# Kernel optimization log

Hardware: AMD Instinct MI355X
Metric: run time of the kernel (lower is better)

Reference implementation:

```python
import jax, jax.numpy as jnp
import numpy as np

B, T, C, H = 4, 2048, 1024, 16
HS = C // H  # head size 64
LN_EPS = 1e-5


def setup_inputs() -> dict:
    key = jax.random.key(0)
    ks = jax.random.split(key, 14)
    s = lambda fan_in: 1.0 / np.sqrt(fan_in)
    return {
        "x": jax.random.normal(ks[0], (B, T, C), jnp.float32),
        # weights stored [in, out] (transposed vs torch nn.Linear) for y = x @ W + b
        "c_attn_w": jax.random.normal(ks[1], (C, 3 * C), jnp.float32) * s(C),
        "c_attn_b": jnp.zeros((3 * C,), jnp.float32),
        "c_proj_w": jax.random.normal(ks[2], (C, C), jnp.float32) * s(C),
        "c_proj_b": jnp.zeros((C,), jnp.float32),
        "fc_w": jax.random.normal(ks[3], (C, 4 * C), jnp.float32) * s(C),
        "fc_b": jnp.zeros((4 * C,), jnp.float32),
        "proj_w": jax.random.normal(ks[4], (4 * C, C), jnp.float32) * s(4 * C),
        "proj_b": jnp.zeros((C,), jnp.float32),
        "ln1_g": jnp.ones((C,), jnp.float32),
        "ln1_b": jnp.zeros((C,), jnp.float32),
        "ln2_g": jnp.ones((C,), jnp.float32),
        "ln2_b": jnp.zeros((C,), jnp.float32),
    }


def layer_norm(x, g, b):
    mu = jnp.mean(x, axis=-1, keepdims=True)
    var = jnp.var(x, axis=-1, keepdims=True)
    return (x - mu) * jax.lax.rsqrt(var + LN_EPS) * g + b


def attention(x, c_attn_w, c_attn_b, c_proj_w, c_proj_b):
    Bs, Ts, Cs = x.shape
    qkv = x @ c_attn_w + c_attn_b  # (B,T,3C)
    q, k, v = jnp.split(qkv, 3, axis=-1)
    q = q.reshape(Bs, Ts, H, HS).transpose(0, 2, 1, 3)  # (B,H,T,hs)
    k = k.reshape(Bs, Ts, H, HS).transpose(0, 2, 1, 3)
    v = v.reshape(Bs, Ts, H, HS).transpose(0, 2, 1, 3)
    wei = jnp.einsum("bhqd,bhkd->bhqk", q, k) * (1.0 / np.sqrt(HS))
    causal = jnp.tril(jnp.ones((Ts, Ts), bool))
    wei = jnp.where(causal, wei, -jnp.inf)
    wei = jax.nn.softmax(wei, axis=-1)
    out = jnp.einsum("bhqk,bhkd->bhqd", wei, v)
    out = out.transpose(0, 2, 1, 3).reshape(Bs, Ts, Cs)
    return out @ c_proj_w + c_proj_b


def mlp(x, fc_w, fc_b, proj_w, proj_b):
    h = jax.nn.gelu(x @ fc_w + fc_b, approximate=True)
    return h @ proj_w + proj_b


def reference(x, c_attn_w, c_attn_b, c_proj_w, c_proj_b, fc_w, fc_b, proj_w, proj_b, ln1_g, ln1_b, ln2_g, ln2_b):
    x = x + attention(layer_norm(x, ln1_g, ln1_b), c_attn_w, c_attn_b, c_proj_w, c_proj_b)
    out = x + mlp(layer_norm(x, ln2_g, ln2_b), fc_w, fc_b, proj_w, proj_b)
    return out
```

## Files before the change

### kernel.cpp

```cpp
#include <hip/hip_runtime.h>

typedef unsigned short u16;
typedef __attribute__((ext_vector_type(8))) short bf16x8;
typedef __attribute__((ext_vector_type(4))) float f32x4;

#define SC_LOG2E 0.18033688011112043f
#define MB_LOG2E 17.31234049066756f

__device__ __forceinline__ float b2f(u16 u) {
  union { unsigned int i; float f; } v; v.i = ((unsigned int)u) << 16; return v.f;
}
__device__ __forceinline__ u16 f2b(float f) {
  unsigned int x = __float_as_uint(f);
  unsigned int r = (x + 0x7fffu + ((x >> 16) & 1u)) >> 16;
  return (u16)r;
}

#define GLOAD_LDS16(g, l)                                                              \
  __builtin_amdgcn_global_load_lds((const __attribute__((address_space(1))) void*)(g), \
                                   (__attribute__((address_space(3))) void*)(l), 16, 0, 0)

__global__ __launch_bounds__(256) void transpose_cast_kernel(const float* __restrict__ in,
                                                             u16* __restrict__ out,
                                                             int K, int N) {
  __shared__ float tile[64][65];
  const int tid = threadIdx.x;
  const int n0 = blockIdx.x * 64, k0 = blockIdx.y * 64;
#pragma unroll
  for (int it = 0; it < 4; ++it) {
    int lin = it * 256 + tid;
    int r = lin >> 4, c4 = (lin & 15) * 4;
    float4 v = *(const float4*)&in[(size_t)(k0 + r) * N + n0 + c4];
    tile[r][c4 + 0] = v.x; tile[r][c4 + 1] = v.y;
    tile[r][c4 + 2] = v.z; tile[r][c4 + 3] = v.w;
  }
  __syncthreads();
#pragma unroll
  for (int it = 0; it < 2; ++it) {
    int lin = it * 256 + tid;
    int r = lin >> 3, c8 = (lin & 7) * 8;
    u16 tmp[8];
#pragma unroll
    for (int j = 0; j < 8; ++j) tmp[j] = f2b(tile[c8 + j][r]);
    *(uint4*)&out[(size_t)(n0 + r) * K + k0 + c8] = *(const uint4*)tmp;
  }
}

__global__ __launch_bounds__(256) void transpose_v_kernel(const u16* __restrict__ qkv,
                                                          u16* __restrict__ vt) {
  __shared__ float tl[64][65];
  const int tid = threadIdx.x;
  const int bh = blockIdx.y, b = bh >> 4, h = bh & 15;
  const int t0 = blockIdx.x * 64;
  const int voff = 2048 + h * 64;
#pragma unroll
  for (int it = 0; it < 2; ++it) {
    int lin = it * 256 + tid;
    int tt = lin >> 3, d8 = (lin & 7) * 8;
    uint4 v = *(const uint4*)&qkv[((size_t)b * 2048 + t0 + tt) * 3072 + voff + d8];
    const u16* p = (const u16*)&v;
#pragma unroll
    for (int j = 0; j < 8; ++j) tl[tt][d8 + j] = b2f(p[j]);
  }
  __syncthreads();
#pragma unroll
  for (int it = 0; it < 2; ++it) {
    int lin = it * 256 + tid;
    int d = lin >> 3, t8 = (lin & 7) * 8;
    u16 tmp[8];
#pragma unroll
    for (int j = 0; j < 8; ++j) tmp[j] = f2b(tl[t8 + j][d]);
    *(uint4*)&vt[((size_t)bh * 64 + d) * 2048 + t0 + t8] = *(const uint4*)tmp;
  }
}

template <bool INF32>
__global__ __launch_bounds__(256) void ln_kernel(const void* __restrict__ xv,
                                                 const float* __restrict__ g,
                                                 const float* __restrict__ b,
                                                 u16* __restrict__ o, int C) {
  const int row = blockIdx.x, tid = threadIdx.x;
  const int wave = tid >> 6, lane = tid & 63;
  const int base = tid * 4;
  float f[4];
  if (INF32) {
    float4 v = *(const float4*)((const float*)xv + (size_t)row * C + base);
    f[0] = v.x; f[1] = v.y; f[2] = v.z; f[3] = v.w;
  } else {
    ushort4 v = *(const ushort4*)((const u16*)xv + (size_t)row * C + base);
    f[0] = b2f(v.x); f[1] = b2f(v.y); f[2] = b2f(v.z); f[3] = b2f(v.w);
  }
  float s = f[0] + f[1] + f[2] + f[3];
  float q = f[0] * f[0] + f[1] * f[1] + f[2] * f[2] + f[3] * f[3];
#pragma unroll
  for (int off = 1; off < 64; off <<= 1) {
    s += __shfl_xor(s, off);
    q += __shfl_xor(q, off);
  }
  __shared__ float reds[4], redq[4];
  if (lane == 0) { reds[wave] = s; redq[wave] = q; }
  __syncthreads();
  float S = reds[0] + reds[1] + reds[2] + reds[3];
  float Q = redq[0] + redq[1] + redq[2] + redq[3];
  const float inv = 1.0f / (float)C;
  float mean = S * inv;
  float var = Q * inv - mean * mean;
  float rs = rsqrtf(var + 1e-5f);
  float4 gv = *(const float4*)&g[base];
  float4 bv = *(const float4*)&b[base];
  ushort4 ov;
  ov.x = f2b((f[0] - mean) * rs * gv.x + bv.x);
  ov.y = f2b((f[1] - mean) * rs * gv.y + bv.y);
  ov.z = f2b((f[2] - mean) * rs * gv.z + bv.z);
  ov.w = f2b((f[3] - mean) * rs * gv.w + bv.w);
  *(ushort4*)&o[(size_t)row * C + base] = ov;
}

__device__ __forceinline__ float gelu_fn(float v) {
  float a = 0.7978845608028654f * __builtin_fmaf(0.044715f * v * v, v, v);
  float t = __builtin_amdgcn_exp2f(a * -2.8853900817779268f);
  return v * __builtin_amdgcn_rcpf(1.0f + t);
}

template <bool GELU, int RESMODE, bool OUTF32>
__global__ __launch_bounds__(256) void gemm_kernel(const u16* __restrict__ A,
                                                   const u16* __restrict__ Bt,
                                                   const float* __restrict__ bias,
                                                   const void* __restrict__ res,
                                                   void* __restrict__ Cv,
                                                   int M, int N, int K) {
  __shared__ u16 As[128 * 64];
  __shared__ u16 Bs[128 * 64];
  const int tid = threadIdx.x;
  const int wave = tid >> 6, lane = tid & 63;
  const int lhi = lane >> 4, llo = lane & 15;
  const int sw = llo & 7;
  const int m0 = blockIdx.x * 128, n0 = blockIdx.y * 128;
  const int wr = (wave >> 1) * 64, wc = (wave & 1) * 64;

  f32x4 acc[4][4] = {};

  for (int k0 = 0; k0 < K; k0 += 64) {
#pragma unroll
    for (int p = 0; p < 4; ++p) {
      int s = p * 256 + tid;
      int r = s >> 3;
      int c = ((s & 7) ^ (r & 7)) * 8;
      GLOAD_LDS16(A + (size_t)(m0 + r) * K + k0 + c, As + s * 8);
      GLOAD_LDS16(Bt + (size_t)(n0 + r) * K + k0 + c, Bs + s * 8);
    }
    __syncthreads();
#pragma unroll
    for (int kk = 0; kk < 2; ++kk) {
      const int cp = ((kk * 4 + lhi) ^ sw) * 8;
      bf16x8 af[4], bf[4];
#pragma unroll
      for (int i = 0; i < 4; ++i)
        af[i] = *(const bf16x8*)&As[(wr + i * 16 + llo) * 64 + cp];
#pragma unroll
      for (int j = 0; j < 4; ++j)
        bf[j] = *(const bf16x8*)&Bs[(wc + j * 16 + llo) * 64 + cp];
#pragma unroll
      for (int i = 0; i < 4; ++i)
#pragma unroll
        for (int j = 0; j < 4; ++j)
          acc[i][j] = __builtin_amdgcn_mfma_f32_16x16x32_bf16(af[i], bf[j], acc[i][j], 0, 0, 0);
    }
    __syncthreads();
  }

#pragma unroll
  for (int i = 0; i < 4; ++i) {
    int row = m0 + wr + i * 16 + lhi * 4;
#pragma unroll
    for (int j = 0; j < 4; ++j) {
      int col = n0 + wc + j * 16 + llo;
      float bv = bias[col];
#pragma unroll
      for (int r = 0; r < 4; ++r) {
        float v = acc[i][j][r] + bv;
        if (GELU) v = gelu_fn(v);
        size_t idx = (size_t)(row + r) * N + col;
        if (RESMODE == 1) v += b2f(((const u16*)res)[idx]);
        if (RESMODE == 2) v += ((const float*)res)[idx];
        if (OUTF32) ((float*)Cv)[idx] = v;
        else ((u16*)Cv)[idx] = f2b(v);
      }
    }
  }
}

template <bool GELU>
__global__ __launch_bounds__(512, 2) void gemm256_kernel(const u16* __restrict__ A,
                                                         const u16* __restrict__ Bt,
                                                         const float* __restrict__ bias,
                                                         u16* __restrict__ Cv,
                                                         int M, int N, int K) {
  __shared__ u16 As[2][256 * 64];
  __shared__ u16 Bs[2][256 * 64];
  const int tid = threadIdx.x;
  const int wave = tid >> 6, lane = tid & 63;
  const int lhi = lane >> 4, llo = lane & 15;
  const int sw = llo & 7;
  const int m0 = blockIdx.x * 256, n0 = blockIdx.y * 256;
  const int wr = (wave >> 2) * 128, wc = (wave & 3) * 64;

  f32x4 acc[8][4] = {};
  const int nkt = K >> 6;

  auto stage = [&](int b, int kt) {
    const int k0 = kt * 64;
#pragma unroll
    for (int p = 0; p < 4; ++p) {
      int s = p * 512 + tid;
      int r = s >> 3;
      int c = ((s & 7) ^ (r & 7)) * 8;
      GLOAD_LDS16(A + (size_t)(m0 + r) * K + k0 + c, &As[b][s * 8]);
      GLOAD_LDS16(Bt + (size_t)(n0 + r) * K + k0 + c, &Bs[b][s * 8]);
    }
  };

  stage(0, 0);
  stage(1, 1);
  asm volatile("s_waitcnt vmcnt(8)" ::: "memory");
  __builtin_amdgcn_s_barrier();

  int cur = 0;
  for (int kt = 0; kt < nkt; ++kt) {
#pragma unroll
    for (int kk = 0; kk < 2; ++kk) {
      const int cp = ((kk * 4 + lhi) ^ sw) * 8;
      bf16x8 af[8], bf[4];
#pragma unroll
      for (int i = 0; i < 8; ++i)
        af[i] = *(const bf16x8*)&As[cur][(wr + i * 16 + llo) * 64 + cp];
#pragma unroll
      for (int j = 0; j < 4; ++j)
        bf[j] = *(const bf16x8*)&Bs[cur][(wc + j * 16 + llo) * 64 + cp];
      __builtin_amdgcn_s_setprio(1);
#pragma unroll
      for (int i = 0; i < 8; ++i)
#pragma unroll
        for (int j = 0; j < 4; ++j)
          acc[i][j] = __builtin_amdgcn_mfma_f32_16x16x32_bf16(af[i], bf[j], acc[i][j], 0, 0, 0);
      __builtin_amdgcn_s_setprio(0);
    }
    asm volatile("s_waitcnt lgkmcnt(0)" ::: "memory");
    __builtin_amdgcn_s_barrier();
    if (kt + 2 < nkt) {
      stage(cur, kt + 2);
      asm volatile("s_waitcnt vmcnt(8)" ::: "memory");
      __builtin_amdgcn_s_barrier();
    } else if (kt + 1 < nkt) {
      asm volatile("s_waitcnt vmcnt(0)" ::: "memory");
      __builtin_amdgcn_s_barrier();
    }
    cur ^= 1;
  }

#pragma unroll
  for (int i = 0; i < 8; ++i) {
    int row = m0 + wr + i * 16 + lhi * 4;
#pragma unroll
    for (int j = 0; j < 4; ++j) {
      int col = n0 + wc + j * 16 + llo;
      float bv = bias[col];
#pragma unroll
      for (int r = 0; r < 4; ++r) {
        float v = acc[i][j][r] + bv;
        if (GELU) v = gelu_fn(v);
        Cv[(size_t)(row + r) * N + col] = f2b(v);
      }
    }
  }
}

__global__ __launch_bounds__(512, 4) void attn_kernel(const u16* __restrict__ qkv,
                                                      const u16* __restrict__ vt,
                                                      u16* __restrict__ out) {
  __shared__ u16 Ks[64 * 68];
  __shared__ u16 Vs[64 * 68];
  __shared__ u16 Ps[128 * 68];
  const int tid = threadIdx.x;
  const int wave = tid >> 6, lane = tid & 63;
  const int lhi = lane >> 4, llo = lane & 15;
  const int pr = blockIdx.x;
  const int bh = blockIdx.y;
  const int b = bh >> 4, h = bh & 15;
  const size_t rowbase = (size_t)b * 2048;
  const int qoff = h * 64, koff = 1024 + h * 64;
  const u16* vtb = vt + (size_t)bh * 64 * 2048;
  const int sr = tid >> 3;
  const int sc = (tid & 7) * 8;

#pragma unroll
  for (int ph = 0; ph < 2; ++ph) {
    const int qtile = ph ? pr : (15 - pr);
    const int q0 = qtile * 128;
    const int qrow = q0 + wave * 16;

    bf16x8 qf[2];
#pragma unroll
    for (int kk = 0; kk < 2; ++kk) {
      uint4 v = *(const uint4*)&qkv[(rowbase + qrow + llo) * 3072 + qoff + kk * 32 + lhi * 8];
      qf[kk] = *(const bf16x8*)&v;
    }

    f32x4 oacc[4] = {};
    float l_st[4] = {};
    const int nkt = 2 * qtile + 2;

    uint4 pk = *(const uint4*)&qkv[(rowbase + sr) * 3072 + koff + sc];
    uint4 pv = *(const uint4*)&vtb[(size_t)sr * 2048 + sc];

    for (int kt = 0; kt < nkt; ++kt) {
      const int kt0 = kt * 64;
      __syncthreads();
      *(uint4*)&Ks[sr * 68 + sc] = pk;
      *(uint4*)&Vs[sr * 68 + sc] = pv;
      __syncthreads();
      if (kt + 1 < nkt) {
        const int nt0 = kt0 + 64;
        pk = *(const uint4*)&qkv[(rowbase + nt0 + sr) * 3072 + koff + sc];
        pv = *(const uint4*)&vtb[(size_t)sr * 2048 + nt0 + sc];
      }

      if (kt0 > qrow + 15) continue;

      f32x4 s[4] = {};
#pragma unroll
      for (int kk = 0; kk < 2; ++kk)
#pragma unroll
        for (int j = 0; j < 4; ++j) {
          bf16x8 kf = *(const bf16x8*)&Ks[(j * 16 + llo) * 68 + kk * 32 + lhi * 8];
          s[j] = __builtin_amdgcn_mfma_f32_16x16x32_bf16(qf[kk], kf, s[j], 0, 0, 0);
        }

      const bool msk = (kt0 + 63 > qrow);
      u16* psrow = &Ps[(wave * 16) * 68];
#pragma unroll
      for (int j = 0; j < 4; ++j) {
        const int key = kt0 + j * 16 + llo;
#pragma unroll
        for (int r = 0; r < 4; ++r) {
          float sv = s[j][r];
          if (msk) sv = (key <= qrow + lhi * 4 + r) ? sv : -1e30f;
          float p = __builtin_amdgcn_exp2f(__builtin_fmaf(sv, SC_LOG2E, -MB_LOG2E));
          l_st[r] += p;
          psrow[(lhi * 4 + r) * 68 + j * 16 + llo] = (u16)(__float_as_uint(p) >> 16);
        }
      }

#pragma unroll
      for (int kc = 0; kc < 2; ++kc) {
        bf16x8 pf = *(const bf16x8*)&Ps[(wave * 16 + llo) * 68 + kc * 32 + lhi * 8];
#pragma unroll
        for (int j4 = 0; j4 < 4; ++j4) {
          bf16x8 vf = *(const bf16x8*)&Vs[(j4 * 16 + llo) * 68 + kc * 32 + lhi * 8];
          oacc[j4] = __builtin_amdgcn_mfma_f32_16x16x32_bf16(pf, vf, oacc[j4], 0, 0, 0);
        }
      }
    }

#pragma unroll
    for (int r = 0; r < 4; ++r) {
      float v = l_st[r];
      v += __shfl_xor(v, 1);
      v += __shfl_xor(v, 2);
      v += __shfl_xor(v, 4);
      v += __shfl_xor(v, 8);
      l_st[r] = 1.0f / v;
    }
#pragma unroll
    for (int j4 = 0; j4 < 4; ++j4)
#pragma unroll
      for (int r = 0; r < 4; ++r) {
        size_t row = rowbase + qrow + lhi * 4 + r;
        out[row * 1024 + h * 64 + j4 * 16 + llo] = f2b(oacc[j4][r] * l_st[r]);
      }
  }
}

extern "C" void kernel_launch(void* const* d_in, const int* in_sizes, int n_in,
                              void* d_out, int out_size, void* d_ws, size_t ws_size,
                              hipStream_t stream) {
  const float* x        = (const float*)d_in[0];
  const float* c_attn_w = (const float*)d_in[1];
  const float* c_attn_b = (const float*)d_in[2];
  const float* c_proj_w = (const float*)d_in[3];
  const float* c_proj_b = (const float*)d_in[4];
  const float* fc_w     = (const float*)d_in[5];
  const float* fc_b     = (const float*)d_in[6];
  const float* proj_w   = (const float*)d_in[7];
  const float* proj_b   = (const float*)d_in[8];
  const float* ln1_g    = (const float*)d_in[9];
  const float* ln1_b    = (const float*)d_in[10];
  const float* ln2_g    = (const float*)d_in[11];
  const float* ln2_b    = (const float*)d_in[12];
  float* out = (float*)d_out;
  u16* ws = (u16*)d_ws;

  const size_t M = 8192;
  u16* ln_buf = ws;
  u16* qkv    = ln_buf + M * 1024;
  u16* x1     = qkv + M * 3072;
  u16* hbuf   = x1 + M * 1024;
  u16* wT_a   = hbuf + M * 4096;
  u16* wT_p   = wT_a + 3072 * 1024;
  u16* wT_f   = wT_p + 1024 * 1024;
  u16* wT_m   = wT_f + 4096 * 1024;
  u16* vt     = hbuf;

  dim3 blk(256);
  transpose_cast_kernel<<<dim3(48, 16), blk, 0, stream>>>(c_attn_w, wT_a, 1024, 3072);
  transpose_cast_kernel<<<dim3(16, 16), blk, 0, stream>>>(c_proj_w, wT_p, 1024, 1024);
  transpose_cast_kernel<<<dim3(64, 16), blk, 0, stream>>>(fc_w, wT_f, 1024, 4096);
  transpose_cast_kernel<<<dim3(16, 64), blk, 0, stream>>>(proj_w, wT_m, 4096, 1024);

  ln_kernel<true><<<8192, blk, 0, stream>>>(x, ln1_g, ln1_b, ln_buf, 1024);
  gemm256_kernel<false><<<dim3(32, 12), dim3(512), 0, stream>>>(ln_buf, wT_a, c_attn_b, qkv, 8192, 3072, 1024);
  transpose_v_kernel<<<dim3(32, 64), blk, 0, stream>>>(qkv, vt);
  attn_kernel<<<dim3(8, 64), dim3(512), 0, stream>>>(qkv, vt, ln_buf);
  gemm_kernel<false, 2, false><<<dim3(64, 8), blk, 0, stream>>>(ln_buf, wT_p, c_proj_b, x, x1, 8192, 1024, 1024);
  ln_kernel<false><<<8192, blk, 0, stream>>>(x1, ln2_g, ln2_b, ln_buf, 1024);
  gemm256_kernel<true><<<dim3(32, 16), dim3(512), 0, stream>>>(ln_buf, wT_f, fc_b, hbuf, 8192, 4096, 1024);
  gemm_kernel<false, 1, true><<<dim3(64, 8), blk, 0, stream>>>(hbuf, wT_m, proj_b, x1, out, 8192, 1024, 4096);
}
```

Baseline: 482.1 us.

## Split GEMM k-tile into four quadrant phases interleaving LDS reads, prefetch and MFMA

```diff
diff --git a/kernel.cpp b/kernel.cpp
--- a/kernel.cpp
+++ b/kernel.cpp
@@ -19,6 +19,10 @@
 #define GLOAD_LDS16(g, l)                                                              \
   __builtin_amdgcn_global_load_lds((const __attribute__((address_space(1))) void*)(g), \
                                    (__attribute__((address_space(3))) void*)(l), 16, 0, 0)
+
+#define ASM_VMCNT8() asm volatile("s_waitcnt vmcnt(8)" ::: "memory")
+#define ASM_VMCNT0() asm volatile("s_waitcnt vmcnt(0)" ::: "memory")
+#define ASM_LGKM0() asm volatile("s_waitcnt lgkmcnt(0)" ::: "memory")
 
 __global__ __launch_bounds__(256) void transpose_cast_kernel(const float* __restrict__ in,
                                                              u16* __restrict__ out,
@@ -204,57 +208,123 @@
   const int sw = llo & 7;
   const int m0 = blockIdx.x * 256, n0 = blockIdx.y * 256;
   const int wr = (wave >> 2) * 128, wc = (wave & 3) * 64;
+  const int srow = tid >> 3, schunk = tid & 7;
 
   f32x4 acc[8][4] = {};
   const int nkt = K >> 6;
 
-  auto stage = [&](int b, int kt) {
-    const int k0 = kt * 64;
-#pragma unroll
-    for (int p = 0; p < 4; ++p) {
-      int s = p * 512 + tid;
-      int r = s >> 3;
-      int c = ((s & 7) ^ (r & 7)) * 8;
-      GLOAD_LDS16(A + (size_t)(m0 + r) * K + k0 + c, &As[b][s * 8]);
-      GLOAD_LDS16(Bt + (size_t)(n0 + r) * K + k0 + c, &Bs[b][s * 8]);
-    }
+  auto stageA = [&](int b, int kt, int g) {
+    int r = g * 64 + srow;
+    int c = (schunk ^ (r & 7)) * 8;
+    GLOAD_LDS16(A + (size_t)(m0 + r) * K + kt * 64 + c, &As[b][r * 64 + schunk * 8]);
   };
-
-  stage(0, 0);
-  stage(1, 1);
-  asm volatile("s_waitcnt vmcnt(8)" ::: "memory");
+  auto stageB = [&](int b, int kt, int g) {
+    int r = g * 64 + srow;
+    int c = (schunk ^ (r & 7)) * 8;
+    GLOAD_LDS16(Bt + (size_t)(n0 + r) * K + kt * 64 + c, &Bs[b][r * 64 + schunk * 8]);
+  };
+  auto stageTile = [&](int b, int kt) {
+#pragma unroll
+    for (int g = 0; g < 4; ++g) stageA(b, kt, g);
+#pragma unroll
+    for (int g = 0; g < 4; ++g) stageB(b, kt, g);
+  };
+
+  stageTile(0, 0);
+  stageTile(1, 1);
+  ASM_VMCNT8();
   __builtin_amdgcn_s_barrier();
 
   int cur = 0;
   for (int kt = 0; kt < nkt; ++kt) {
-#pragma unroll
-    for (int kk = 0; kk < 2; ++kk) {
-      const int cp = ((kk * 4 + lhi) ^ sw) * 8;
-      bf16x8 af[8], bf[4];
-#pragma unroll
-      for (int i = 0; i < 8; ++i)
-        af[i] = *(const bf16x8*)&As[cur][(wr + i * 16 + llo) * 64 + cp];
-#pragma unroll
-      for (int j = 0; j < 4; ++j)
-        bf[j] = *(const bf16x8*)&Bs[cur][(wc + j * 16 + llo) * 64 + cp];
-      __builtin_amdgcn_s_setprio(1);
-#pragma unroll
-      for (int i = 0; i < 8; ++i)
-#pragma unroll
-        for (int j = 0; j < 4; ++j)
-          acc[i][j] = __builtin_amdgcn_mfma_f32_16x16x32_bf16(af[i], bf[j], acc[i][j], 0, 0, 0);
-      __builtin_amdgcn_s_setprio(0);
-    }
-    asm volatile("s_waitcnt lgkmcnt(0)" ::: "memory");
-    __builtin_amdgcn_s_barrier();
-    if (kt + 2 < nkt) {
-      stage(cur, kt + 2);
-      asm volatile("s_waitcnt vmcnt(8)" ::: "memory");
-      __builtin_amdgcn_s_barrier();
+    const int pf = kt + 2;
+    const bool do_pf = pf < nkt;
+    const u16* as = As[cur];
+    const u16* bs = Bs[cur];
+
+    bf16x8 alo[4][2], blo[2][2], bhi[2][2], ahi[4][2];
+#pragma unroll
+    for (int i = 0; i < 4; ++i)
+#pragma unroll
+      for (int kq = 0; kq < 2; ++kq)
+        alo[i][kq] = *(const bf16x8*)&as[(wr + i * 16 + llo) * 64 + (((kq * 4 + lhi) ^ sw) * 8)];
+#pragma unroll
+    for (int j = 0; j < 2; ++j)
+#pragma unroll
+      for (int kq = 0; kq < 2; ++kq)
+        blo[j][kq] = *(const bf16x8*)&bs[(wc + j * 16 + llo) * 64 + (((kq * 4 + lhi) ^ sw) * 8)];
+    __builtin_amdgcn_s_barrier();
+    ASM_LGKM0();
+    __builtin_amdgcn_s_setprio(1);
+#pragma unroll
+    for (int i = 0; i < 4; ++i)
+#pragma unroll
+      for (int j = 0; j < 2; ++j)
+#pragma unroll
+        for (int kq = 0; kq < 2; ++kq)
+          acc[i][j] = __builtin_amdgcn_mfma_f32_16x16x32_bf16(alo[i][kq], blo[j][kq], acc[i][j], 0, 0, 0);
+    __builtin_amdgcn_s_setprio(0);
+    __builtin_amdgcn_s_barrier();
+
+#pragma unroll
+    for (int j = 0; j < 2; ++j)
+#pragma unroll
+      for (int kq = 0; kq < 2; ++kq)
+        bhi[j][kq] = *(const bf16x8*)&bs[(wc + (j + 2) * 16 + llo) * 64 + (((kq * 4 + lhi) ^ sw) * 8)];
+    if (do_pf) { stageA(cur, pf, 0); stageA(cur, pf, 2); }
+    __builtin_amdgcn_s_barrier();
+    ASM_LGKM0();
+    __builtin_amdgcn_s_setprio(1);
+#pragma unroll
+    for (int i = 0; i < 4; ++i)
+#pragma unroll
+      for (int j = 0; j < 2; ++j)
+#pragma unroll
+        for (int kq = 0; kq < 2; ++kq)
+          acc[i][j + 2] = __builtin_amdgcn_mfma_f32_16x16x32_bf16(alo[i][kq], bhi[j][kq], acc[i][j + 2], 0, 0, 0);
+    __builtin_amdgcn_s_setprio(0);
+    __builtin_amdgcn_s_barrier();
+
+#pragma unroll
+    for (int i = 0; i < 4; ++i)
+#pragma unroll
+      for (int kq = 0; kq < 2; ++kq)
+        ahi[i][kq] = *(const bf16x8*)&as[(wr + (i + 4) * 16 + llo) * 64 + (((kq * 4 + lhi) ^ sw) * 8)];
+    if (do_pf) {
+#pragma unroll
+      for (int g = 0; g < 4; ++g) stageB(cur, pf, g);
+    }
+    __builtin_amdgcn_s_barrier();
+    ASM_LGKM0();
+    __builtin_amdgcn_s_setprio(1);
+#pragma unroll
+    for (int i = 0; i < 4; ++i)
+#pragma unroll
+      for (int j = 0; j < 2; ++j)
+#pragma unroll
+        for (int kq = 0; kq < 2; ++kq)
+          acc[i + 4][j] = __builtin_amdgcn_mfma_f32_16x16x32_bf16(ahi[i][kq], blo[j][kq], acc[i + 4][j], 0, 0, 0);
+    __builtin_amdgcn_s_setprio(0);
+    __builtin_amdgcn_s_barrier();
+
+    if (do_pf) {
+      stageA(cur, pf, 1); stageA(cur, pf, 3);
+      ASM_VMCNT8();
     } else if (kt + 1 < nkt) {
-      asm volatile("s_waitcnt vmcnt(0)" ::: "memory");
-      __builtin_amdgcn_s_barrier();
-    }
+      ASM_VMCNT0();
+    }
+    __builtin_amdgcn_s_barrier();
+    __builtin_amdgcn_s_setprio(1);
+#pragma unroll
+    for (int i = 0; i < 4; ++i)
+#pragma unroll
+      for (int j = 0; j < 2; ++j)
+#pragma unroll
+        for (int kq = 0; kq < 2; ++kq)
+          acc[i + 4][j + 2] = __builtin_amdgcn_mfma_f32_16x16x32_bf16(ahi[i][kq], bhi[j][kq], acc[i + 4][j + 2], 0, 0, 0);
+    __builtin_amdgcn_s_setprio(0);
+    __builtin_amdgcn_s_barrier();
+
     cur ^= 1;
   }
 
```

New measurement: 482.2 us. No clear change (+0.0%).
